# Kernel tuning notes

Hardware: AMD Instinct MI355X
Metric: run time of the kernel (lower is better)

The kernel has to match this reference:

```python
import jax, jax.numpy as jnp
import numpy as np

N, E, F, C, V, L = 40000, 640000, 128, 20, 50000, 3  # nodes, edges, feat, classes, vocab, GEN layers
HID = 2 * F  # GENConv MLP hidden size (PyG: in_channels * 2)
GEN_EPS = 1e-7
LN_EPS = 1e-5


def layer_norm(x, g, b):
    mu = x.mean(-1, keepdims=True)
    var = ((x - mu) ** 2).mean(-1, keepdims=True)
    return (x - mu) * jax.lax.rsqrt(var + LN_EPS) * g + b


def seg_softmax(logits, idx, n):
    # numerically stable per-destination softmax over edges, elementwise per feature
    m = jax.ops.segment_max(logits, idx, num_segments=n)  # [n, F]
    e = jnp.exp(logits - m[idx])
    s = jax.ops.segment_sum(e, idx, num_segments=n)
    return e / (s[idx] + 1e-16)


def gen_conv(x, src, dst, t, w1, b1, g, bn, w2, b2):
    # GENConv (softmax aggr): msg = relu(x_j) + eps; alpha = softmax(t*msg | dst); mlp(x + sum(alpha*msg))
    n = x.shape[0]
    msg = jax.nn.relu(x[src]) + GEN_EPS              # [E, F]
    alpha = seg_softmax(msg * t, dst, n)             # [E, F]
    aggr = jax.ops.segment_sum(msg * alpha, dst, num_segments=n)  # [n, F]
    h = x + aggr
    h = jax.nn.relu(layer_norm(h @ w1 + b1, g, bn))  # MLP: Linear -> LayerNorm -> ReLU
    return h @ w2 + b2                               # final Linear


def gcn_conv(x, src, dst, ew, w, b):
    # GCNConv with self loops + symmetric normalization
    n = x.shape[0]
    loop = jnp.arange(n)
    s2 = jnp.concatenate([src, loop])
    d2 = jnp.concatenate([dst, loop])
    w2_ = jnp.concatenate([ew, jnp.ones((n,), x.dtype)])
    deg = jax.ops.segment_sum(w2_, d2, num_segments=n)
    dis = jnp.where(deg > 0, jax.lax.rsqrt(deg), 0.0)
    norm = dis[s2] * w2_ * dis[d2]                   # [E+n]
    xw = x @ w                                       # [n, C]
    out = jax.ops.segment_sum(norm[:, None] * xw[s2], d2, num_segments=n)
    return out + b


def setup_inputs() -> dict:
    key = jax.random.key(0)
    ks = jax.random.split(key, 16)
    sc_f = 1.0 / np.sqrt(F)
    sc_h = 1.0 / np.sqrt(HID)
    return {
        "x_ids": jax.random.randint(ks[0], (N,), 0, V),
        "edge_index": jax.random.randint(ks[1], (2, E), 0, N),
        "edge_attr": jax.random.uniform(ks[2], (E,), jnp.float32),
        "emb": jax.random.normal(ks[3], (V, F), jnp.float32),
        "ln_g": jnp.ones((L, F), jnp.float32),
        "ln_b": jnp.zeros((L, F), jnp.float32),
        "t": jnp.ones((L,), jnp.float32),
        "w1": jax.random.normal(ks[4], (L, F, HID), jnp.float32) * sc_f,
        "b1": jnp.zeros((L, HID), jnp.float32),
        "mlp_g": jnp.ones((L, HID), jnp.float32),
        "mlp_b": jnp.zeros((L, HID), jnp.float32),
        "w2": jax.random.normal(ks[5], (L, HID, F), jnp.float32) * sc_h,
        "b2": jnp.zeros((L, F), jnp.float32),
        "gcn_w": jax.random.normal(ks[6], (F, C), jnp.float32) * sc_f,
        "gcn_b": jnp.zeros((C,), jnp.float32),
    }


def reference(x_ids, edge_index, edge_attr, emb, ln_g, ln_b, t, w1, b1, mlp_g, mlp_b, w2, b2, gcn_w, gcn_b):
    src, dst = edge_index[0], edge_index[1]
    h = emb[x_ids]  # [N, F]
    for i in range(L):  # DeepGCNLayer res+: x + conv(dropout(act(norm(x)))); dropout=eval (identity)
        xn = jax.nn.relu(layer_norm(h, ln_g[i], ln_b[i]))
        h = h + gen_conv(xn, src, dst, t[i], w1[i], b1[i], mlp_g[i], mlp_b[i], w2[i], b2[i])
    out = gcn_conv(h, src, dst, edge_attr, gcn_w, gcn_b)
    return jax.nn.log_softmax(out, axis=1)
```

## Files before the change

kernel.cpp:

```cpp
#include <hip/hip_runtime.h>
#include <hip/hip_fp16.h>
#include <math.h>

constexpr int Nn  = 40000;
constexpr int Ee  = 640000;
constexpr int Fd  = 128;
constexpr int Hid = 256;
constexpr int Cc  = 20;
constexpr float GEN_EPS = 1e-7f;
constexpr float LN_EPS  = 1e-5f;

using bfrag = __attribute__((ext_vector_type(8))) short;
using f32x4 = __attribute__((ext_vector_type(4))) float;
typedef __attribute__((ext_vector_type(4))) unsigned short us4;

__device__ __forceinline__ unsigned short f2bf(float f) {
  unsigned u = __float_as_uint(f);
  u += 0x7FFF + ((u >> 16) & 1);
  return (unsigned short)(u >> 16);
}

__global__ void zero_int_k(int* __restrict__ p, int n) {
  int i = blockIdx.x * 256 + threadIdx.x;
  if (i < n) p[i] = 0;
}

__global__ void count_k(const int* __restrict__ dst, int* __restrict__ cnt,
                        int* __restrict__ rank) {
  int e = blockIdx.x * 256 + threadIdx.x;
  if (e < Ee) rank[e] = atomicAdd(&cnt[dst[e]], 1);
}

__device__ __forceinline__ int block_incl_scan256(int v) {
  int t = threadIdx.x, lane = t & 63, wid = t >> 6;
  int x = v;
  #pragma unroll
  for (int off = 1; off < 64; off <<= 1) {
    int y = __shfl_up(x, off);
    if (lane >= off) x += y;
  }
  __shared__ int wsum[4];
  if (lane == 63) wsum[wid] = x;
  __syncthreads();
  int add = 0;
  #pragma unroll
  for (int w = 0; w < 4; ++w) if (w < wid) add += wsum[w];
  return x + add;
}

__global__ __launch_bounds__(256) void blocksum_k(const int* __restrict__ cnt,
                                                  int* __restrict__ bsum, int n) {
  int i = blockIdx.x * 256 + threadIdx.x;
  int v = (i < n) ? cnt[i] : 0;
  int lane = threadIdx.x & 63, wid = threadIdx.x >> 6;
  #pragma unroll
  for (int m = 32; m >= 1; m >>= 1) v += __shfl_xor(v, m);
  __shared__ int s4[4];
  if (lane == 0) s4[wid] = v;
  __syncthreads();
  if (threadIdx.x == 0) bsum[blockIdx.x] = s4[0] + s4[1] + s4[2] + s4[3];
}

__global__ __launch_bounds__(256) void scanbsum_k(int* __restrict__ bsum, int nb) {
  int t = threadIdx.x;
  int v = (t < nb) ? bsum[t] : 0;
  int incl = block_incl_scan256(v);
  if (t < nb) bsum[t] = incl - v;
}

__global__ __launch_bounds__(256) void scanfinal_k(const int* __restrict__ cnt,
                                                   const int* __restrict__ bsum,
                                                   int* __restrict__ row_ptr, int n) {
  int b = blockIdx.x, t = threadIdx.x;
  int i = b * 256 + t;
  int v = (i < n) ? cnt[i] : 0;
  int incl = block_incl_scan256(v);
  if (i < n) row_ptr[i + 1] = bsum[b] + incl;
  if (b == 0 && t == 0) row_ptr[0] = 0;
}

__global__ void scatter_k(const int* __restrict__ src, const int* __restrict__ dst,
                          const float* __restrict__ eattr,
                          const int* __restrict__ row_ptr, const int* __restrict__ rank,
                          uint2* __restrict__ cole) {
  int e = blockIdx.x * 256 + threadIdx.x;
  if (e >= Ee) return;
  int d = dst[e];
  int p = row_ptr[d] + rank[e];
  cole[p] = make_uint2((unsigned)src[e], __float_as_uint(eattr[e]));
}

__global__ void deg_dis_k(const int* __restrict__ row_ptr, const uint2* __restrict__ cole,
                          float* __restrict__ dis) {
  int i = blockIdx.x * 256 + threadIdx.x;
  if (i >= Nn) return;
  int b = row_ptr[i], e = row_ptr[i + 1];
  float s = 1.f;
  for (int j = b; j < e; ++j) s += __uint_as_float(cole[j].y);
  dis[i] = (s > 0.f) ? rsqrtf(s) : 0.f;
}

__global__ void prep_w_k(const float* __restrict__ w1, const float* __restrict__ w2,
                         unsigned short* __restrict__ w1h, unsigned short* __restrict__ w2h) {
  int i = blockIdx.x * 256 + threadIdx.x;
  constexpr int TOT = 3 * Fd * Hid;
  if (i >= TOT) return;
  int j = i & 7, l = (i >> 3) & 63, tk = (i >> 9) & 63, layer = i >> 15;
  int k_lo = (l >> 4) * 4 + (j & 3) + 16 * (j >> 2);
  {
    int kc = tk >> 4, tt = tk & 15;
    int k = kc * 32 + k_lo, c = tt * 16 + (l & 15);
    w1h[i] = f2bf(w1[((size_t)layer * Fd + k) * Hid + c]);
  }
  {
    int kc = tk >> 3, tt = tk & 7;
    int k = kc * 32 + k_lo, c = tt * 16 + (l & 15);
    w2h[i] = f2bf(w2[((size_t)layer * Hid + k) * Fd + c]);
  }
}

__global__ __launch_bounds__(256) void embed_ln_k(const int* __restrict__ ids,
                                                  const float* __restrict__ emb,
                                                  const float* __restrict__ g,
                                                  const float* __restrict__ b,
                                                  float* __restrict__ h,
                                                  __half* __restrict__ xnh) {
  int node = blockIdx.x * 4 + (threadIdx.x >> 6);
  int lane = threadIdx.x & 63;
  float2 v = *(const float2*)(emb + (size_t)ids[node] * Fd + lane * 2);
  *(float2*)(h + (size_t)node * Fd + lane * 2) = v;
  float s = v.x + v.y;
  #pragma unroll
  for (int m = 32; m >= 1; m >>= 1) s += __shfl_xor(s, m);
  float mu = s * (1.f / 128.f);
  float d0 = v.x - mu, d1 = v.y - mu;
  float q = d0 * d0 + d1 * d1;
  #pragma unroll
  for (int m = 32; m >= 1; m >>= 1) q += __shfl_xor(q, m);
  float rs = rsqrtf(q * (1.f / 128.f) + LN_EPS);
  float2 gg = *(const float2*)(g + lane * 2);
  float2 bb = *(const float2*)(b + lane * 2);
  float ox = fmaxf(d0 * rs * gg.x + bb.x, 0.f);
  float oy = fmaxf(d1 * rs * gg.y + bb.y, 0.f);
  *(__half2*)(xnh + (size_t)node * Fd + lane * 2) = __floats2half2_rn(ox, oy);
}

__global__ __launch_bounds__(256) void gen_agg_k(const __half* __restrict__ xnh,
                                                 const int* __restrict__ row_ptr,
                                                 const uint2* __restrict__ cole,
                                                 const float* __restrict__ t_ptr,
                                                 unsigned short* __restrict__ h2b) {
  int wid = blockIdx.x * 4 + (threadIdx.x >> 6);
  int lane = threadIdx.x & 63;
  int sub = lane >> 4;
  int node = wid * 4 + sub;
  int f0 = (lane & 15) * 8;
  float t = t_ptr[0];
  int beg = row_ptr[node], end = row_ptr[node + 1];
  const __half* xb = xnh + f0;
  float se[8], sm[8];
  #pragma unroll
  for (int i = 0; i < 8; ++i) { se[i] = 0.f; sm[i] = 0.f; }

  for (int j = beg; j < end; j += 8) {
    int idx[8];
    #pragma unroll
    for (int k = 0; k < 8; ++k) idx[k] = (j + k < end) ? (int)cole[j + k].x : -1;
    uint4 hv[8];
    #pragma unroll
    for (int k = 0; k < 8; ++k)
      if (idx[k] >= 0) hv[k] = *(const uint4*)(xb + (size_t)idx[k] * Fd);
    #pragma unroll
    for (int k = 0; k < 8; ++k) {
      if (idx[k] >= 0) {
        const __half2* hp = (const __half2*)&hv[k];
        #pragma unroll
        for (int q = 0; q < 4; ++q) {
          float2 v = __half22float2(hp[q]);
          float m0 = v.x + GEN_EPS, m1 = v.y + GEN_EPS;
          float e0 = __expf(t * m0), e1 = __expf(t * m1);
          se[2 * q]     += e0;  se[2 * q + 1] += e1;
          sm[2 * q]      = fmaf(m0, e0, sm[2 * q]);
          sm[2 * q + 1]  = fmaf(m1, e1, sm[2 * q + 1]);
        }
      }
    }
  }

  uint4 sv = *(const uint4*)(xb + (size_t)node * Fd);
  const __half2* sp2 = (const __half2*)&sv;
  unsigned short ob[8];
  #pragma unroll
  for (int q = 0; q < 4; ++q) {
    float2 sf = __half22float2(sp2[q]);
    ob[2 * q]     = f2bf(sf.x + sm[2 * q]     / (se[2 * q]     + 1e-16f));
    ob[2 * q + 1] = f2bf(sf.y + sm[2 * q + 1] / (se[2 * q + 1] + 1e-16f));
  }
  *(uint4*)(h2b + (size_t)node * Fd + f0) = *(uint4*)ob;
}

__global__ __launch_bounds__(256) void gemm1m_k(const unsigned short* __restrict__ Az,
                                                const unsigned short* __restrict__ Bhp,
                                                const float* __restrict__ bias,
                                                const float* __restrict__ gam,
                                                const float* __restrict__ bln,
                                                unsigned short* __restrict__ Zb) {
  __shared__ unsigned short Ab[32][136];
  __shared__ float sred[2][32][2];
  const int t = threadIdx.x;
  const int w = t >> 6, l = t & 63;
  const int rg = w & 1, cg = w >> 1;
  const int g4 = l >> 4, cl = l & 15;
  const int r0 = blockIdx.x * 32;

  {
    int row = t >> 3;
    int base = (t & 7) * 16;
    const unsigned short* sp = Az + (size_t)(r0 + row) * Fd + base;
    #pragma unroll
    for (int hb = 0; hb < 2; ++hb) {
      int kk0 = base + hb * 8;
      uint4 a = *(const uint4*)(sp + hb * 8);
      int chunk = kk0 >> 5, ww = kk0 & 31;
      int d = chunk * 32 + 8 * ((ww & 15) >> 2) + 4 * (ww >> 4);
      us4 v0 = {(unsigned short)a.x, (unsigned short)(a.x >> 16),
                (unsigned short)a.y, (unsigned short)(a.y >> 16)};
      us4 v1 = {(unsigned short)a.z, (unsigned short)(a.z >> 16),
                (unsigned short)a.w, (unsigned short)(a.w >> 16)};
      *(us4*)&Ab[row][d] = v0;
      *(us4*)&Ab[row][d + 8] = v1;
    }
  }
  __syncthreads();

  f32x4 acc[8];
  #pragma unroll
  for (int i = 0; i < 8; ++i) acc[i] = (f32x4){0.f, 0.f, 0.f, 0.f};
  for (int kc = 0; kc < 4; ++kc) {
    bfrag ab = *(const bfrag*)&Ab[16 * rg + cl][kc * 32 + g4 * 8];
    const unsigned short* bh = Bhp + ((size_t)(kc * 16 + cg * 8) * 64 + l) * 8;
    #pragma unroll
    for (int tt = 0; tt < 8; ++tt) {
      bfrag vbh = *(const bfrag*)(bh + tt * 512);
      acc[tt] = __builtin_amdgcn_mfma_f32_16x16x32_bf16(ab, vbh, acc[tt], 0, 0, 0);
    }
  }

  float bcol[8], gcol[8], blc[8];
  #pragma unroll
  for (int tt = 0; tt < 8; ++tt) {
    int c = cg * 128 + 16 * tt + cl;
    bcol[tt] = bias[c]; gcol[tt] = gam[c]; blc[tt] = bln[c];
  }
  #pragma unroll
  for (int j = 0; j < 4; ++j) {
    float s = 0.f, q = 0.f;
    #pragma unroll
    for (int tt = 0; tt < 8; ++tt) {
      float x = acc[tt][j] + bcol[tt];
      acc[tt][j] = x;
      s += x;
      q = fmaf(x, x, q);
    }
    #pragma unroll
    for (int m = 8; m >= 1; m >>= 1) { s += __shfl_xor(s, m); q += __shfl_xor(q, m); }
    if (cl == 0) {
      int rl = 16 * rg + 4 * g4 + j;
      sred[cg][rl][0] = s;
      sred[cg][rl][1] = q;
    }
  }
  __syncthreads();
  #pragma unroll
  for (int j = 0; j < 4; ++j) {
    int rl = 16 * rg + 4 * g4 + j;
    float s = sred[0][rl][0] + sred[1][rl][0];
    float q = sred[0][rl][1] + sred[1][rl][1];
    float mu = s * (1.f / 256.f);
    float rs = rsqrtf(q * (1.f / 256.f) - mu * mu + LN_EPS);
    int row = r0 + rl;
    #pragma unroll
    for (int tt = 0; tt < 8; ++tt) {
      float z = fmaxf((acc[tt][j] - mu) * rs * gcol[tt] + blc[tt], 0.f);
      Zb[(size_t)row * Hid + cg * 128 + 16 * tt + cl] = f2bf(z);
    }
  }
}

__global__ __launch_bounds__(256) void gemm2m_k(const unsigned short* __restrict__ Az,
                                                const unsigned short* __restrict__ Bhp,
                                                const float* __restrict__ bias,
                                                float* __restrict__ H,
                                                const float* __restrict__ gam,
                                                const float* __restrict__ bln,
                                                __half* __restrict__ XNh,
                                                const float* __restrict__ gw,
                                                const float* __restrict__ dis,
                                                __half* __restrict__ xwdh,
                                                int mode) {
  __shared__ unsigned short Ab[32][264];
  __shared__ float sred[2][32][2];
  __shared__ float pred[2][32][20];
  __shared__ float gwS[Fd * Cc];
  const int t = threadIdx.x;
  const int w = t >> 6, l = t & 63;
  const int rg = w & 1, cg = w >> 1;
  const int g4 = l >> 4, cl = l & 15;
  const int r0 = blockIdx.x * 32;

  {
    int row = t >> 3;
    int base = (t & 7) * 32;
    const unsigned short* sp = Az + (size_t)(r0 + row) * Hid + base;
    #pragma unroll
    for (int hb = 0; hb < 4; ++hb) {
      int kk0 = base + hb * 8;
      uint4 a = *(const uint4*)(sp + hb * 8);
      int chunk = kk0 >> 5, ww = kk0 & 31;
      int d = chunk * 32 + 8 * ((ww & 15) >> 2) + 4 * (ww >> 4);
      us4 v0 = {(unsigned short)a.x, (unsigned short)(a.x >> 16),
                (unsigned short)a.y, (unsigned short)(a.y >> 16)};
      us4 v1 = {(unsigned short)a.z, (unsigned short)(a.z >> 16),
                (unsigned short)a.w, (unsigned short)(a.w >> 16)};
      *(us4*)&Ab[row][d] = v0;
      *(us4*)&Ab[row][d + 8] = v1;
    }
  }
  if (mode == 2) {
    for (int i = t; i < Fd * Cc; i += 256) gwS[i] = gw[i];
  }
  __syncthreads();

  f32x4 acc[4];
  #pragma unroll
  for (int i = 0; i < 4; ++i) acc[i] = (f32x4){0.f, 0.f, 0.f, 0.f};
  for (int kf = 0; kf < 8; ++kf) {
    bfrag ab = *(const bfrag*)&Ab[16 * rg + cl][kf * 32 + g4 * 8];
    const unsigned short* bh = Bhp + ((size_t)(kf * 8 + cg * 4) * 64 + l) * 8;
    #pragma unroll
    for (int tt = 0; tt < 4; ++tt) {
      bfrag vbh = *(const bfrag*)(bh + tt * 512);
      acc[tt] = __builtin_amdgcn_mfma_f32_16x16x32_bf16(ab, vbh, acc[tt], 0, 0, 0);
    }
  }

  float bcol[4], gcol[4], blc[4];
  #pragma unroll
  for (int tt = 0; tt < 4; ++tt) {
    int c = cg * 64 + 16 * tt + cl;
    bcol[tt] = bias[c];
    if (mode == 0) { gcol[tt] = gam[c]; blc[tt] = bln[c]; }
  }

  if (mode == 0) {
    #pragma unroll
    for (int j = 0; j < 4; ++j) {
      int row = r0 + 16 * rg + 4 * g4 + j;
      float s = 0.f, q = 0.f;
      #pragma unroll
      for (int tt = 0; tt < 4; ++tt) {
        size_t off = (size_t)row * Fd + cg * 64 + 16 * tt + cl;
        float hv = H[off] + acc[tt][j] + bcol[tt];
        H[off] = hv;
        acc[tt][j] = hv;
        s += hv;
        q = fmaf(hv, hv, q);
      }
      #pragma unroll
      for (int m = 8; m >= 1; m >>= 1) { s += __shfl_xor(s, m); q += __shfl_xor(q, m); }
      if (cl == 0) {
        int rl = 16 * rg + 4 * g4 + j;
        sred[cg][rl][0] = s;
        sred[cg][rl][1] = q;
      }
    }
    __syncthreads();
    #pragma unroll
    for (int j = 0; j < 4; ++j) {
      int rl = 16 * rg + 4 * g4 + j;
      float s = sred[0][rl][0] + sred[1][rl][0];
      float q = sred[0][rl][1] + sred[1][rl][1];
      float mu = s * (1.f / 128.f);
      float rs = rsqrtf(q * (1.f / 128.f) - mu * mu + LN_EPS);
      int row = r0 + rl;
      #pragma unroll
      for (int tt = 0; tt < 4; ++tt) {
        float z = fmaxf((acc[tt][j] - mu) * rs * gcol[tt] + blc[tt], 0.f);
        XNh[(size_t)row * Fd + cg * 64 + 16 * tt + cl] = __float2half_rn(z);
      }
    }
  } else {
    #pragma unroll
    for (int j = 0; j < 4; ++j) {
      int row = r0 + 16 * rg + 4 * g4 + j;
      float p[Cc];
      #pragma unroll
      for (int c = 0; c < Cc; ++c) p[c] = 0.f;
      #pragma unroll
      for (int tt = 0; tt < 4; ++tt) {
        size_t off = (size_t)row * Fd + cg * 64 + 16 * tt + cl;
        float xv = H[off] + acc[tt][j] + bcol[tt];
        const float* wr = &gwS[(cg * 64 + 16 * tt + cl) * Cc];
        #pragma unroll
        for (int c = 0; c < Cc; ++c) p[c] = fmaf(xv, wr[c], p[c]);
      }
      #pragma unroll
      for (int c = 0; c < Cc; ++c) {
        #pragma unroll
        for (int m = 8; m >= 1; m >>= 1) p[c] += __shfl_xor(p[c], m);
      }
      int rl = 16 * rg + 4 * g4 + j;
      if (cl < 10) {
        pred[cg][rl][2 * cl]     = p[2 * cl];
        pred[cg][rl][2 * cl + 1] = p[2 * cl + 1];
      }
    }
    __syncthreads();
    if (cg == 0) {
      #pragma unroll
      for (int j = 0; j < 4; ++j) {
        int rl = 16 * rg + 4 * g4 + j;
        int row = r0 + rl;
        float dvr = dis[row];
        if (cl < 10) {
          float v0 = (pred[0][rl][2 * cl]     + pred[1][rl][2 * cl])     * dvr;
          float v1 = (pred[0][rl][2 * cl + 1] + pred[1][rl][2 * cl + 1]) * dvr;
          *(__half2*)(xwdh + (size_t)row * 32 + 2 * cl) = __floats2half2_rn(v0, v1);
        }
      }
    }
  }
}

__global__ __launch_bounds__(256) void gcn_out_k(const __half* __restrict__ xwdh,
                                                 const int* __restrict__ row_ptr,
                                                 const uint2* __restrict__ cole,
                                                 const float* __restrict__ dis,
                                                 const float* __restrict__ bias,
                                                 float* __restrict__ out) {
  int node = blockIdx.x * 4 + (threadIdx.x >> 6);
  int lane = threadIdx.x & 63;
  int grp = lane / Cc, c = lane % Cc;
  float dv = dis[node];
  float acc = 0.f;
  int beg = row_ptr[node], end = row_ptr[node + 1];
  if (grp < 3) {
    for (int j = beg + grp; j < end; j += 3) {
      uint2 ce = cole[j];
      acc += __uint_as_float(ce.y) * __half2float(xwdh[(size_t)ce.x * 32 + c]);
    }
  }
  int l20 = lane + 20 < 64 ? lane + 20 : lane;
  int l40 = lane + 40 < 64 ? lane + 40 : lane;
  float tot = acc + __shfl(acc, l20) + __shfl(acc, l40);
  float val = 0.f;
  if (lane < Cc)
    val = dv * tot + dv * __half2float(xwdh[(size_t)node * 32 + c]) + bias[c];
  float red = (lane < Cc) ? val : -INFINITY;
  #pragma unroll
  for (int m = 32; m >= 1; m >>= 1) red = fmaxf(red, __shfl_xor(red, m));
  float ex = (lane < Cc) ? __expf(val - red) : 0.f;
  #pragma unroll
  for (int m = 32; m >= 1; m >>= 1) ex += __shfl_xor(ex, m);
  float ls = __logf(ex);
  if (lane < Cc) out[(size_t)node * Cc + c] = val - red - ls;
}

extern "C" void kernel_launch(void* const* d_in, const int* in_sizes, int n_in,
                              void* d_out, int out_size, void* d_ws, size_t ws_size,
                              hipStream_t stream) {
  const int*   x_ids = (const int*)d_in[0];
  const int*   ei    = (const int*)d_in[1];
  const int*   srcp  = ei;
  const int*   dstp  = ei + Ee;
  const float* eattr = (const float*)d_in[2];
  const float* emb   = (const float*)d_in[3];
  const float* ln_g  = (const float*)d_in[4];
  const float* ln_b  = (const float*)d_in[5];
  const float* tpar  = (const float*)d_in[6];
  const float* w1    = (const float*)d_in[7];
  const float* b1    = (const float*)d_in[8];
  const float* mg    = (const float*)d_in[9];
  const float* mb    = (const float*)d_in[10];
  const float* w2    = (const float*)d_in[11];
  const float* b2    = (const float*)d_in[12];
  const float* gw    = (const float*)d_in[13];
  const float* gb    = (const float*)d_in[14];
  float* out = (float*)d_out;

  char* ws = (char*)d_ws;
  float* h    = (float*)ws;  ws += (size_t)Nn * Fd * 4;
  __half* xnh = (__half*)ws; ws += (size_t)Nn * Fd * 2;
  __half* xwdh = (__half*)ws; ws += (size_t)Nn * 32 * 2;
  float* dis  = (float*)ws;  ws += (size_t)Nn * 4;
  unsigned short* h2b = (unsigned short*)ws; ws += (size_t)Nn * Fd * 2;
  unsigned short* z1b = (unsigned short*)ws; ws += (size_t)Nn * Hid * 2;
  unsigned short* w1h = (unsigned short*)ws; ws += (size_t)3 * Fd * Hid * 2;
  unsigned short* w2h = (unsigned short*)ws; ws += (size_t)3 * Fd * Hid * 2;
  int* row_ptr = (int*)ws; ws += (size_t)(Nn + 16) * 4;
  int* cnt   = (int*)ws;   ws += (size_t)Nn * 4;
  int* rank  = (int*)ws;   ws += (size_t)Ee * 4;
  uint2* cole = (uint2*)ws; ws += (size_t)Ee * 8;
  int* bsum  = (int*)ws;   ws += 256 * 4;
  if ((size_t)(ws - (char*)d_ws) > ws_size) return;

  constexpr int NB = (Nn + 255) / 256;

  prep_w_k<<<(3 * Fd * Hid + 255) / 256, 256, 0, stream>>>(w1, w2, w1h, w2h);

  zero_int_k<<<NB, 256, 0, stream>>>(cnt, Nn);
  count_k<<<2500, 256, 0, stream>>>(dstp, cnt, rank);
  blocksum_k<<<NB, 256, 0, stream>>>(cnt, bsum, Nn);
  scanbsum_k<<<1, 256, 0, stream>>>(bsum, NB);
  scanfinal_k<<<NB, 256, 0, stream>>>(cnt, bsum, row_ptr, Nn);
  scatter_k<<<2500, 256, 0, stream>>>(srcp, dstp, eattr, row_ptr, rank, cole);
  deg_dis_k<<<NB, 256, 0, stream>>>(row_ptr, cole, dis);

  embed_ln_k<<<Nn / 4, 256, 0, stream>>>(x_ids, emb, ln_g, ln_b, h, xnh);

  for (int i = 0; i < 3; ++i) {
    gen_agg_k<<<Nn / 16, 256, 0, stream>>>(xnh, row_ptr, cole, tpar + i, h2b);
    gemm1m_k<<<Nn / 32, 256, 0, stream>>>(h2b,
        w1h + (size_t)i * Fd * Hid,
        b1 + i * Hid, mg + i * Hid, mb + i * Hid, z1b);
    gemm2m_k<<<Nn / 32, 256, 0, stream>>>(z1b,
        w2h + (size_t)i * Fd * Hid,
        b2 + i * Fd, h,
        ln_g + (i + 1) * Fd, ln_b + (i + 1) * Fd,
        xnh, gw, dis, xwdh, (i < 2) ? 0 : 2);
  }

  gcn_out_k<<<Nn / 4, 256, 0, stream>>>(xwdh, row_ptr, cole, dis, gb, out);
}
```

Measured before the change: 300.2 us.

## Fuse the two MLP GEMMs into one kernel, keeping hidden activations in LDS

Merges the first GEMM (with LayerNorm and ReLU) and the second GEMM (with residual add and the next LayerNorm or GCN projection) into one kernel per layer. The 256-wide hidden activation stays in shared memory in the MFMA-friendly permuted layout instead of round-tripping through a global bf16 buffer. This removes a global write and read of about 20 MB per layer and one launch per layer. In exchange it uses more LDS per block, which may lower occupancy.

After: 278.0 us (median of 2 runs). 7.4% less time.

```diff
diff --git a/kernel.cpp b/kernel.cpp
--- a/kernel.cpp
+++ b/kernel.cpp
@@ -199,19 +199,21 @@
   *(uint4*)(h2b + (size_t)node * Fd + f0) = *(uint4*)ob;
 }
 
-__global__ __launch_bounds__(256) void gemm1m_k(const unsigned short* __restrict__ Az,
-                                                const unsigned short* __restrict__ Bhp,
-                                                const float* __restrict__ bias,
-                                                const float* __restrict__ gam,
-                                                const float* __restrict__ bln,
-                                                unsigned short* __restrict__ Zb) {
-  __shared__ unsigned short Ab[32][136];
-  __shared__ float sred[2][32][2];
+__device__ __forceinline__ void mlp_core(const unsigned short* __restrict__ Az,
+                                         const unsigned short* __restrict__ W1h,
+                                         const float* __restrict__ b1,
+                                         const float* __restrict__ g1,
+                                         const float* __restrict__ bl1,
+                                         const unsigned short* __restrict__ W2h,
+                                         int r0,
+                                         unsigned short (*Ab)[136],
+                                         unsigned short (*Zl)[264],
+                                         float (*sred)[32][2],
+                                         f32x4* acc2) {
   const int t = threadIdx.x;
   const int w = t >> 6, l = t & 63;
   const int rg = w & 1, cg = w >> 1;
   const int g4 = l >> 4, cl = l & 15;
-  const int r0 = blockIdx.x * 32;
 
   {
     int row = t >> 3;
@@ -238,7 +240,7 @@
   for (int i = 0; i < 8; ++i) acc[i] = (f32x4){0.f, 0.f, 0.f, 0.f};
   for (int kc = 0; kc < 4; ++kc) {
     bfrag ab = *(const bfrag*)&Ab[16 * rg + cl][kc * 32 + g4 * 8];
-    const unsigned short* bh = Bhp + ((size_t)(kc * 16 + cg * 8) * 64 + l) * 8;
+    const unsigned short* bh = W1h + ((size_t)(kc * 16 + cg * 8) * 64 + l) * 8;
     #pragma unroll
     for (int tt = 0; tt < 8; ++tt) {
       bfrag vbh = *(const bfrag*)(bh + tt * 512);
@@ -250,7 +252,7 @@
   #pragma unroll
   for (int tt = 0; tt < 8; ++tt) {
     int c = cg * 128 + 16 * tt + cl;
-    bcol[tt] = bias[c]; gcol[tt] = gam[c]; blc[tt] = bln[c];
+    bcol[tt] = b1[c]; gcol[tt] = g1[c]; blc[tt] = bl1[c];
   }
   #pragma unroll
   for (int j = 0; j < 4; ++j) {
@@ -278,27 +280,109 @@
     float q = sred[0][rl][1] + sred[1][rl][1];
     float mu = s * (1.f / 256.f);
     float rs = rsqrtf(q * (1.f / 256.f) - mu * mu + LN_EPS);
-    int row = r0 + rl;
     #pragma unroll
     for (int tt = 0; tt < 8; ++tt) {
       float z = fmaxf((acc[tt][j] - mu) * rs * gcol[tt] + blc[tt], 0.f);
-      Zb[(size_t)row * Hid + cg * 128 + 16 * tt + cl] = f2bf(z);
-    }
-  }
-}
-
-__global__ __launch_bounds__(256) void gemm2m_k(const unsigned short* __restrict__ Az,
-                                                const unsigned short* __restrict__ Bhp,
-                                                const float* __restrict__ bias,
-                                                float* __restrict__ H,
-                                                const float* __restrict__ gam,
-                                                const float* __restrict__ bln,
-                                                __half* __restrict__ XNh,
-                                                const float* __restrict__ gw,
-                                                const float* __restrict__ dis,
-                                                __half* __restrict__ xwdh,
-                                                int mode) {
-  __shared__ unsigned short Ab[32][264];
+      int d = (cl & 3) + 8 * (cl >> 2) + 4 * (tt & 1) + 32 * ((tt >> 1) + 4 * cg);
+      Zl[rl][d] = f2bf(z);
+    }
+  }
+  __syncthreads();
+
+  #pragma unroll
+  for (int i = 0; i < 4; ++i) acc2[i] = (f32x4){0.f, 0.f, 0.f, 0.f};
+  for (int kf = 0; kf < 8; ++kf) {
+    bfrag ab = *(const bfrag*)&Zl[16 * rg + cl][kf * 32 + g4 * 8];
+    const unsigned short* bh = W2h + ((size_t)(kf * 8 + cg * 4) * 64 + l) * 8;
+    #pragma unroll
+    for (int tt = 0; tt < 4; ++tt) {
+      bfrag vbh = *(const bfrag*)(bh + tt * 512);
+      acc2[tt] = __builtin_amdgcn_mfma_f32_16x16x32_bf16(ab, vbh, acc2[tt], 0, 0, 0);
+    }
+  }
+}
+
+__global__ __launch_bounds__(256) void mlp0_k(const unsigned short* __restrict__ Az,
+                                              const unsigned short* __restrict__ W1h,
+                                              const float* __restrict__ b1,
+                                              const float* __restrict__ g1,
+                                              const float* __restrict__ bl1,
+                                              const unsigned short* __restrict__ W2h,
+                                              const float* __restrict__ b2,
+                                              float* __restrict__ H,
+                                              const float* __restrict__ gN,
+                                              const float* __restrict__ blN,
+                                              __half* __restrict__ XNh) {
+  __shared__ unsigned short Ab[32][136];
+  __shared__ unsigned short Zl[32][264];
+  __shared__ float sred[2][32][2];
+  const int t = threadIdx.x;
+  const int w = t >> 6, l = t & 63;
+  const int rg = w & 1, cg = w >> 1;
+  const int g4 = l >> 4, cl = l & 15;
+  const int r0 = blockIdx.x * 32;
+
+  f32x4 acc2[4];
+  mlp_core(Az, W1h, b1, g1, bl1, W2h, r0, Ab, Zl, sred, acc2);
+
+  float bcol[4], gcol[4], blc[4];
+  #pragma unroll
+  for (int tt = 0; tt < 4; ++tt) {
+    int c = cg * 64 + 16 * tt + cl;
+    bcol[tt] = b2[c];
+    gcol[tt] = gN[c]; blc[tt] = blN[c];
+  }
+  #pragma unroll
+  for (int j = 0; j < 4; ++j) {
+    int row = r0 + 16 * rg + 4 * g4 + j;
+    float s = 0.f, q = 0.f;
+    #pragma unroll
+    for (int tt = 0; tt < 4; ++tt) {
+      size_t off = (size_t)row * Fd + cg * 64 + 16 * tt + cl;
+      float hv = H[off] + acc2[tt][j] + bcol[tt];
+      H[off] = hv;
+      acc2[tt][j] = hv;
+      s += hv;
+      q = fmaf(hv, hv, q);
+    }
+    #pragma unroll
+    for (int m = 8; m >= 1; m >>= 1) { s += __shfl_xor(s, m); q += __shfl_xor(q, m); }
+    if (cl == 0) {
+      int rl = 16 * rg + 4 * g4 + j;
+      sred[cg][rl][0] = s;
+      sred[cg][rl][1] = q;
+    }
+  }
+  __syncthreads();
+  #pragma unroll
+  for (int j = 0; j < 4; ++j) {
+    int rl = 16 * rg + 4 * g4 + j;
+    float s = sred[0][rl][0] + sred[1][rl][0];
+    float q = sred[0][rl][1] + sred[1][rl][1];
+    float mu = s * (1.f / 128.f);
+    float rs = rsqrtf(q * (1.f / 128.f) - mu * mu + LN_EPS);
+    int row = r0 + rl;
+    #pragma unroll
+    for (int tt = 0; tt < 4; ++tt) {
+      float z = fmaxf((acc2[tt][j] - mu) * rs * gcol[tt] + blc[tt], 0.f);
+      XNh[(size_t)row * Fd + cg * 64 + 16 * tt + cl] = __float2half_rn(z);
+    }
+  }
+}
+
+__global__ __launch_bounds__(256) void mlp2_k(const unsigned short* __restrict__ Az,
+                                              const unsigned short* __restrict__ W1h,
+                                              const float* __restrict__ b1,
+                                              const float* __restrict__ g1,
+                                              const float* __restrict__ bl1,
+                                              const unsigned short* __restrict__ W2h,
+                                              const float* __restrict__ b2,
+                                              const float* __restrict__ H,
+                                              const float* __restrict__ gw,
+                                              const float* __restrict__ dis,
+                                              __half* __restrict__ xwdh) {
+  __shared__ unsigned short Ab[32][136];
+  __shared__ unsigned short Zl[32][264];
   __shared__ float sred[2][32][2];
   __shared__ float pred[2][32][20];
   __shared__ float gwS[Fd * Cc];
@@ -308,125 +392,51 @@
   const int g4 = l >> 4, cl = l & 15;
   const int r0 = blockIdx.x * 32;
 
-  {
-    int row = t >> 3;
-    int base = (t & 7) * 32;
-    const unsigned short* sp = Az + (size_t)(r0 + row) * Hid + base;
-    #pragma unroll
-    for (int hb = 0; hb < 4; ++hb) {
-      int kk0 = base + hb * 8;
-      uint4 a = *(const uint4*)(sp + hb * 8);
-      int chunk = kk0 >> 5, ww = kk0 & 31;
-      int d = chunk * 32 + 8 * ((ww & 15) >> 2) + 4 * (ww >> 4);
-      us4 v0 = {(unsigned short)a.x, (unsigned short)(a.x >> 16),
-                (unsigned short)a.y, (unsigned short)(a.y >> 16)};
-      us4 v1 = {(unsigned short)a.z, (unsigned short)(a.z >> 16),
-                (unsigned short)a.w, (unsigned short)(a.w >> 16)};
-      *(us4*)&Ab[row][d] = v0;
-      *(us4*)&Ab[row][d + 8] = v1;
-    }
-  }
-  if (mode == 2) {
-    for (int i = t; i < Fd * Cc; i += 256) gwS[i] = gw[i];
-  }
-  __syncthreads();
-
-  f32x4 acc[4];
-  #pragma unroll
-  for (int i = 0; i < 4; ++i) acc[i] = (f32x4){0.f, 0.f, 0.f, 0.f};
-  for (int kf = 0; kf < 8; ++kf) {
-    bfrag ab = *(const bfrag*)&Ab[16 * rg + cl][kf * 32 + g4 * 8];
-    const unsigned short* bh = Bhp + ((size_t)(kf * 8 + cg * 4) * 64 + l) * 8;
+  for (int i = t; i < Fd * Cc; i += 256) gwS[i] = gw[i];
+
+  f32x4 acc2[4];
+  mlp_core(Az, W1h, b1, g1, bl1, W2h, r0, Ab, Zl, sred, acc2);
+
+  float bcol[4];
+  #pragma unroll
+  for (int tt = 0; tt < 4; ++tt) bcol[tt] = b2[cg * 64 + 16 * tt + cl];
+
+  #pragma unroll
+  for (int j = 0; j < 4; ++j) {
+    int row = r0 + 16 * rg + 4 * g4 + j;
+    float p[Cc];
+    #pragma unroll
+    for (int c = 0; c < Cc; ++c) p[c] = 0.f;
     #pragma unroll
     for (int tt = 0; tt < 4; ++tt) {
-      bfrag vbh = *(const bfrag*)(bh + tt * 512);
-      acc[tt] = __builtin_amdgcn_mfma_f32_16x16x32_bf16(ab, vbh, acc[tt], 0, 0, 0);
-    }
-  }
-
-  float bcol[4], gcol[4], blc[4];
-  #pragma unroll
-  for (int tt = 0; tt < 4; ++tt) {
-    int c = cg * 64 + 16 * tt + cl;
-    bcol[tt] = bias[c];
-    if (mode == 0) { gcol[tt] = gam[c]; blc[tt] = bln[c]; }
-  }
-
-  if (mode == 0) {
-    #pragma unroll
-    for (int j = 0; j < 4; ++j) {
-      int row = r0 + 16 * rg + 4 * g4 + j;
-      float s = 0.f, q = 0.f;
+      size_t off = (size_t)row * Fd + cg * 64 + 16 * tt + cl;
+      float xv = H[off] + acc2[tt][j] + bcol[tt];
+      const float* wr = &gwS[(cg * 64 + 16 * tt + cl) * Cc];
       #pragma unroll
-      for (int tt = 0; tt < 4; ++tt) {
-        size_t off = (size_t)row * Fd + cg * 64 + 16 * tt + cl;
-        float hv = H[off] + acc[tt][j] + bcol[tt];
-        H[off] = hv;
-        acc[tt][j] = hv;
-        s += hv;
-        q = fmaf(hv, hv, q);
-      }
+      for (int c = 0; c < Cc; ++c) p[c] = fmaf(xv, wr[c], p[c]);
+    }
+    #pragma unroll
+    for (int c = 0; c < Cc; ++c) {
       #pragma unroll
-      for (int m = 8; m >= 1; m >>= 1) { s += __shfl_xor(s, m); q += __shfl_xor(q, m); }
-      if (cl == 0) {
-        int rl = 16 * rg + 4 * g4 + j;
-        sred[cg][rl][0] = s;
-        sred[cg][rl][1] = q;
-      }
-    }
-    __syncthreads();
+      for (int m = 8; m >= 1; m >>= 1) p[c] += __shfl_xor(p[c], m);
+    }
+    int rl = 16 * rg + 4 * g4 + j;
+    if (cl < 10) {
+      pred[cg][rl][2 * cl]     = p[2 * cl];
+      pred[cg][rl][2 * cl + 1] = p[2 * cl + 1];
+    }
+  }
+  __syncthreads();
+  if (cg == 0) {
     #pragma unroll
     for (int j = 0; j < 4; ++j) {
       int rl = 16 * rg + 4 * g4 + j;
-      float s = sred[0][rl][0] + sred[1][rl][0];
-      float q = sred[0][rl][1] + sred[1][rl][1];
-      float mu = s * (1.f / 128.f);
-      float rs = rsqrtf(q * (1.f / 128.f) - mu * mu + LN_EPS);
       int row = r0 + rl;
-      #pragma unroll
-      for (int tt = 0; tt < 4; ++tt) {
-        float z = fmaxf((acc[tt][j] - mu) * rs * gcol[tt] + blc[tt], 0.f);
-        XNh[(size_t)row * Fd + cg * 64 + 16 * tt + cl] = __float2half_rn(z);
-      }
-    }
-  } else {
-    #pragma unroll
-    for (int j = 0; j < 4; ++j) {
-      int row = r0 + 16 * rg + 4 * g4 + j;
-      float p[Cc];
-      #pragma unroll
-      for (int c = 0; c < Cc; ++c) p[c] = 0.f;
-      #pragma unroll
-      for (int tt = 0; tt < 4; ++tt) {
-        size_t off = (size_t)row * Fd + cg * 64 + 16 * tt + cl;
-        float xv = H[off] + acc[tt][j] + bcol[tt];
-        const float* wr = &gwS[(cg * 64 + 16 * tt + cl) * Cc];
-        #pragma unroll
-        for (int c = 0; c < Cc; ++c) p[c] = fmaf(xv, wr[c], p[c]);
-      }
-      #pragma unroll
-      for (int c = 0; c < Cc; ++c) {
-        #pragma unroll
-        for (int m = 8; m >= 1; m >>= 1) p[c] += __shfl_xor(p[c], m);
-      }
-      int rl = 16 * rg + 4 * g4 + j;
+      float dvr = dis[row];
       if (cl < 10) {
-        pred[cg][rl][2 * cl]     = p[2 * cl];
-        pred[cg][rl][2 * cl + 1] = p[2 * cl + 1];
-      }
-    }
-    __syncthreads();
-    if (cg == 0) {
-      #pragma unroll
-      for (int j = 0; j < 4; ++j) {
-        int rl = 16 * rg + 4 * g4 + j;
-        int row = r0 + rl;
-        float dvr = dis[row];
-        if (cl < 10) {
-          float v0 = (pred[0][rl][2 * cl]     + pred[1][rl][2 * cl])     * dvr;
-          float v1 = (pred[0][rl][2 * cl + 1] + pred[1][rl][2 * cl + 1]) * dvr;
-          *(__half2*)(xwdh + (size_t)row * 32 + 2 * cl) = __floats2half2_rn(v0, v1);
-        }
+        float v0 = (pred[0][rl][2 * cl]     + pred[1][rl][2 * cl])     * dvr;
+        float v1 = (pred[0][rl][2 * cl + 1] + pred[1][rl][2 * cl + 1]) * dvr;
+        *(__half2*)(xwdh + (size_t)row * 32 + 2 * cl) = __floats2half2_rn(v0, v1);
       }
     }
   }
@@ -494,7 +504,6 @@
   __half* xwdh = (__half*)ws; ws += (size_t)Nn * 32 * 2;
   float* dis  = (float*)ws;  ws += (size_t)Nn * 4;
   unsigned short* h2b = (unsigned short*)ws; ws += (size_t)Nn * Fd * 2;
-  unsigned short* z1b = (unsigned short*)ws; ws += (size_t)Nn * Hid * 2;
   unsigned short* w1h = (unsigned short*)ws; ws += (size_t)3 * Fd * Hid * 2;
   unsigned short* w2h = (unsigned short*)ws; ws += (size_t)3 * Fd * Hid * 2;
   int* row_ptr = (int*)ws; ws += (size_t)(Nn + 16) * 4;
@@ -520,14 +529,19 @@
 
   for (int i = 0; i < 3; ++i) {
     gen_agg_k<<<Nn / 16, 256, 0, stream>>>(xnh, row_ptr, cole, tpar + i, h2b);
-    gemm1m_k<<<Nn / 32, 256, 0, stream>>>(h2b,
-        w1h + (size_t)i * Fd * Hid,
-        b1 + i * Hid, mg + i * Hid, mb + i * Hid, z1b);
-    gemm2m_k<<<Nn / 32, 256, 0, stream>>>(z1b,
-        w2h + (size_t)i * Fd * Hid,
-        b2 + i * Fd, h,
-        ln_g + (i + 1) * Fd, ln_b + (i + 1) * Fd,
-        xnh, gw, dis, xwdh, (i < 2) ? 0 : 2);
+    if (i < 2) {
+      mlp0_k<<<Nn / 32, 256, 0, stream>>>(h2b,
+          w1h + (size_t)i * Fd * Hid,
+          b1 + i * Hid, mg + i * Hid, mb + i * Hid,
+          w2h + (size_t)i * Fd * Hid, b2 + i * Fd, h,
+          ln_g + (i + 1) * Fd, ln_b + (i + 1) * Fd, xnh);
+    } else {
+      mlp2_k<<<Nn / 32, 256, 0, stream>>>(h2b,
+          w1h + (size_t)i * Fd * Hid,
+          b1 + i * Hid, mg + i * Hid, mb + i * Hid,
+          w2h + (size_t)i * Fd * Hid, b2 + i * Fd, h,
+          gw, dis, xwdh);
+    }
   }
 
   gcn_out_k<<<Nn / 4, 256, 0, stream>>>(xwdh, row_ptr, cole, dis, gb, out);
```
